# Optimization experiments

Hardware: AMD Instinct MI355X
Metric: run time of the kernel (lower is better)

The kernel has to match this reference:

```python
import jax, jax.numpy as jnp
import numpy as np

N, A, C = 4, 8732, 81
SCALE_XY, SCALE_WH = 0.1, 0.2   # dboxes.scale_xy / scale_wh; Loss uses reciprocals
LAM, W_IOU = 1.0, 0.01
EPS_IOU = float(np.finfo(float).eps)


def setup_inputs() -> dict:
    key = jax.random.key(0)
    ks = jax.random.split(key, 8)
    ploc = jax.random.normal(ks[0], (N, 4, A), dtype=jnp.float32) * 0.5
    plabel = jax.random.normal(ks[1], (N, C, A), dtype=jnp.float32)
    # ground-truth loc in xywh with strictly positive wh (loc_vec takes a log)
    gxy = jax.random.uniform(ks[2], (N, 2, A), dtype=jnp.float32)
    gwh = jax.random.uniform(ks[3], (N, 2, A), dtype=jnp.float32) * 0.4 + 0.05
    gloc = jnp.concatenate([gxy, gwh], axis=1)
    lab = jax.random.randint(ks[4], (N, A), 1, C)
    keep = jax.random.uniform(ks[5], (N, A)) < 0.02
    glabel = jnp.where(keep, lab, 0).astype(jnp.int32)
    # default boxes in xywh, shape [1, 4, A]
    dxy = jax.random.uniform(ks[6], (1, 2, A), dtype=jnp.float32)
    dwh = jax.random.uniform(ks[7], (1, 2, A), dtype=jnp.float32) * 0.45 + 0.05
    dboxes = jnp.concatenate([dxy, dwh], axis=1)
    return {"ploc": ploc, "plabel": plabel, "gloc": gloc, "glabel": glabel, "dboxes": dboxes}


def _decode_ltrb(loc, dboxes):
    """scale_back_batch: encoded [N,4,A] + dboxes xywh [1,4,A] -> ltrb [N,A,4]."""
    b = jnp.transpose(loc, (0, 2, 1))      # [N, A, 4]
    d = jnp.transpose(dboxes, (0, 2, 1))   # [1, A, 4]
    xy = SCALE_XY * b[..., :2] * d[..., 2:] + d[..., :2]
    wh = jnp.exp(SCALE_WH * b[..., 2:]) * d[..., 2:]
    return jnp.concatenate([xy - 0.5 * wh, xy + 0.5 * wh], axis=-1)


def _iou_sum(p, g):
    """p, g: [A,4] ltrb -> per-anchor sum over all g boxes of IoU(p_i, g_k)."""
    area_p = (p[:, 2] - p[:, 0]) * (p[:, 3] - p[:, 1])
    area_g = (g[:, 2] - g[:, 0]) * (g[:, 3] - g[:, 1])
    iw = jnp.maximum(jnp.minimum(p[:, None, 2], g[None, :, 2]) - jnp.maximum(p[:, None, 0], g[None, :, 0]), 0.0)
    ih = jnp.maximum(jnp.minimum(p[:, None, 3], g[None, :, 3]) - jnp.maximum(p[:, None, 1], g[None, :, 1]), 0.0)
    inter = iw * ih                                      # [A, A]
    ua = jnp.maximum(area_p[:, None] + area_g[None, :] - inter, EPS_IOU)
    return (inter / ua).sum(axis=1)                      # [A]


def _forward(ploc, plabel, gloc, glabel, dboxes):
    mask = glabel > 0                                    # [N, A]
    pos_num = mask.sum(axis=1)                           # [N]

    # loc_vec: encode ground truth against default boxes
    dxy, dwh = dboxes[:, :2, :], dboxes[:, 2:, :]
    gxy_t = (1.0 / SCALE_XY) * (gloc[:, :2, :] - dxy) / dwh
    gwh_t = (1.0 / SCALE_WH) * jnp.log(gloc[:, 2:, :] / dwh)
    vec_gd = jnp.concatenate([gxy_t, gwh_t], axis=1)     # [N, 4, A]

    # SmoothL1 (beta=1), summed over coord dim
    diff = ploc - vec_gd
    ad = jnp.abs(diff)
    sl1 = jnp.where(ad < 1.0, 0.5 * diff * diff, ad - 0.5).sum(axis=1)  # [N, A]

    # per-anchor cross entropy
    logp = jax.nn.log_softmax(plabel, axis=1)            # [N, C, A]
    con = -jnp.take_along_axis(logp, glabel[:, None, :], axis=1)[:, 0, :]  # [N, A]

    # weighted-IoU reweighting (weights are detached in the original)
    p_ltrb = _decode_ltrb(ploc, dboxes)                  # [N, A, 4]
    g_ltrb = _decode_ltrb(gloc, dboxes)
    iou_s = jax.vmap(_iou_sum)(p_ltrb, g_ltrb)           # [N, A]
    valid = (p_ltrb[..., 0] < p_ltrb[..., 2]) & (p_ltrb[..., 1] < p_ltrb[..., 3])
    weights = jnp.where(valid, W_IOU * iou_s ** LAM, 0.0)
    weights = jax.lax.stop_gradient(weights)
    sl1 = (sl1 / (sl1 + weights)) * sl1

    sl1_pos = (mask.astype(sl1.dtype) * sl1).sum(axis=1)  # [N]

    # hard negative mining: double argsort for ranks
    con_neg = jnp.where(mask, 0.0, con)
    con_idx = jnp.argsort(-con_neg, axis=1)
    con_rank = jnp.argsort(con_idx, axis=1)
    neg_num = jnp.minimum(3 * pos_num, A)[:, None]
    neg_mask = con_rank < neg_num
    closs = (con * (mask.astype(con.dtype) + neg_mask.astype(con.dtype))).sum(axis=1)

    total = sl1_pos + closs
    num_mask = (pos_num > 0).astype(total.dtype)
    pn = jnp.maximum(pos_num.astype(total.dtype), 1e-6)
    return (total * num_mask / pn).mean()


def reference(ploc, plabel, gloc, glabel, dboxes):
    return _forward(ploc, plabel, gloc, glabel, dboxes)
```

## Files before the change

kernel.cpp:

```cpp
#include <hip/hip_runtime.h>
#include <math.h>

#define A_N 8732
#define A4 2183
#define NAT (4 * A_N)
#define BATCH 4
#define CLS 81
#define TILE 256
#define NBINS 2048
#define HB 16
#define HCHUNK ((A_N + HB - 1) / HB)
#define CSPL 8
#define PLB 8

__device__ __forceinline__ float sl1f(float d) {
    float ad = fabsf(d);
    return ad < 1.0f ? 0.5f * d * d : ad - 0.5f;
}
__device__ __forceinline__ float fget(const float4& v, int j) {
    switch (j) { case 0: return v.x; case 1: return v.y; case 2: return v.z; default: return v.w; }
}
__device__ __forceinline__ unsigned umap(float v) {
    return __float_as_uint(v) | 0x80000000u;
}

__device__ void suffix_find(const int* lcnt, const float* lsum, int k, int tid,
                            int* ic, float* fsum,
                            int* o_b, int* o_krem, float* o_sumA)
{
    int base = tid * 8;
    int cs = 0; float ss = 0.0f;
    #pragma unroll
    for (int j = 0; j < 8; j++) { cs += lcnt[base + j]; ss += lsum[base + j]; }
    ic[tid] = cs; fsum[tid] = ss;
    __syncthreads();
    for (int off = 1; off < TILE; off <<= 1) {
        int v = ic[tid]; float f = fsum[tid];
        int v2 = 0; float f2 = 0.0f;
        if (tid + off < TILE) { v2 = ic[tid + off]; f2 = fsum[tid + off]; }
        __syncthreads();
        ic[tid] = v + v2; fsum[tid] = f + f2;
        __syncthreads();
    }
    int run = ic[tid] - cs;
    float runs = fsum[tid] - ss;
    for (int j = 7; j >= 0; j--) {
        int b = base + j; int c = lcnt[b];
        if (run < k && run + c >= k) { *o_b = b; *o_krem = k - run; *o_sumA = runs; }
        run += c; runs += lsum[b];
    }
    __syncthreads();
}

__global__ void init_kernel(int* h1cnt, float* h1sum, int* h2cnt, float* h2sum,
                            int* posnum, float* sums, float* out) {
    int idx = blockIdx.x * TILE + threadIdx.x;
    const int HN = BATCH * NBINS;
    if (idx < HN) { h1cnt[idx] = 0; h1sum[idx] = 0.0f; h2cnt[idx] = 0; h2sum[idx] = 0.0f; }
    if (idx < BATCH) posnum[idx] = 0;
    if (idx < 2 * BATCH) sums[idx] = 0.0f;
    if (idx == 0) out[0] = 0.0f;
}

__global__ __launch_bounds__(TILE) void prep_kernel(
    const float* __restrict__ ploc, const float* __restrict__ plabel,
    const float* __restrict__ gloc, const int* __restrict__ glabel,
    const float* __restrict__ dboxes,
    float4* __restrict__ pbox, float4* __restrict__ gbox,
    float4* __restrict__ sl1raw4, float* __restrict__ xg,
    float* __restrict__ separt,
    int* __restrict__ poslist, int* __restrict__ posnum)
{
    int a4 = blockIdx.x * TILE + threadIdx.x;
    int n = blockIdx.y, z = blockIdx.z;
    if (a4 >= A4) return;

    if (z < CSPL) {
        int c0 = z * 10, c1 = (z == CSPL - 1) ? CLS : c0 + 10;
        const float4* pb4 = (const float4*)plabel + (size_t)n * CLS * A4;
        float4 se = make_float4(0.f, 0.f, 0.f, 0.f);
        for (int c = c0; c < c1; c++) {
            float4 v = pb4[(size_t)c * A4 + a4];
            se.x += expf(v.x); se.y += expf(v.y); se.z += expf(v.z); se.w += expf(v.w);
        }
        ((float4*)(separt + (size_t)z * NAT + (size_t)n * A_N))[a4] = se;
        return;
    }

    const float4* pl4 = (const float4*)ploc + (size_t)n * 4 * A4;
    const float4* gl4 = (const float4*)gloc + (size_t)n * 4 * A4;
    const float4* db4 = (const float4*)dboxes;
    const int4*   lb4 = (const int4*)glabel + (size_t)n * A4;

    float4 dx = db4[0*A4+a4], dy = db4[1*A4+a4], dw = db4[2*A4+a4], dh = db4[3*A4+a4];
    float4 px = pl4[0*A4+a4], py = pl4[1*A4+a4], pw = pl4[2*A4+a4], ph = pl4[3*A4+a4];
    float4 gx = gl4[0*A4+a4], gy = gl4[1*A4+a4], gw = gl4[2*A4+a4], gh = gl4[3*A4+a4];
    int4 lab4 = lb4[a4];
    int labs[4] = {lab4.x, lab4.y, lab4.z, lab4.w};

    float slr[4];
    #pragma unroll
    for (int j = 0; j < 4; j++) {
        int a = 4 * a4 + j;
        float d0 = fget(dx,j), d1 = fget(dy,j), d2 = fget(dw,j), d3 = fget(dh,j);
        float p0 = fget(px,j), p1 = fget(py,j), p2 = fget(pw,j), p3 = fget(ph,j);
        float g0 = fget(gx,j), g1 = fget(gy,j), g2 = fget(gw,j), g3 = fget(gh,j);

        float v0 = 10.0f * (g0 - d0) / d2;
        float v1 = 10.0f * (g1 - d1) / d3;
        float v2 = 5.0f * logf(g2 / d2);
        float v3 = 5.0f * logf(g3 / d3);
        slr[j] = sl1f(p0-v0) + sl1f(p1-v1) + sl1f(p2-v2) + sl1f(p3-v3);

        float cx = 0.1f*p0*d2 + d0, cy = 0.1f*p1*d3 + d1;
        float cw = expf(0.2f*p2)*d2, ch = expf(0.2f*p3)*d3;
        pbox[(size_t)n*A_N + a] = make_float4(cx-0.5f*cw, cy-0.5f*ch, cx+0.5f*cw, cy+0.5f*ch);
        float ex = 0.1f*g0*d2 + d0, ey = 0.1f*g1*d3 + d1;
        float ew = expf(0.2f*g2)*d2, eh = expf(0.2f*g3)*d3;
        gbox[(size_t)n*A_N + a] = make_float4(ex-0.5f*ew, ey-0.5f*eh, ex+0.5f*ew, ey+0.5f*eh);

        int lab = labs[j];
        xg[n*A_N + a] = plabel[(size_t)n*CLS*A_N + (size_t)lab*A_N + a];
        if (lab > 0) {
            int pos = atomicAdd(&posnum[n], 1);
            poslist[n*A_N + pos] = a;
        }
    }
    sl1raw4[(size_t)n*A4 + a4] = make_float4(slr[0], slr[1], slr[2], slr[3]);
}

__global__ __launch_bounds__(TILE) void mid_kernel(
    const float* __restrict__ separt, const float* __restrict__ xg,
    const int* __restrict__ glabel,
    const float4* __restrict__ pbox, const float4* __restrict__ gbox,
    const float* __restrict__ sl1raw, const int* __restrict__ poslist,
    const int* __restrict__ posnum,
    float* __restrict__ conneg, float* __restrict__ sums,
    int* __restrict__ h1cnt, float* __restrict__ h1sum)
{
    __shared__ int   lcnt[NBINS];
    __shared__ float lsum[NBINS];
    __shared__ float r4[4];
    const int n = blockIdx.y, z = blockIdx.z, tid = threadIdx.x;

    if (z == 0) {
        for (int b = tid; b < NBINS; b += TILE) { lcnt[b] = 0; lsum[b] = 0.0f; }
        __syncthreads();
        int i0 = blockIdx.x * HCHUNK, i1 = min(A_N, i0 + HCHUNK);
        for (int i = i0 + tid; i < i1; i += TILE) {
            float se = 0.0f;
            #pragma unroll
            for (int z2 = 0; z2 < CSPL; z2++) se += separt[(size_t)z2 * NAT + n * A_N + i];
            float cv = logf(se) - xg[n * A_N + i];
            bool msk = glabel[n * A_N + i] > 0;
            float cng = msk ? 0.0f : cv;
            conneg[n * A_N + i] = cng;
            if (msk) atomicAdd(&sums[n], cv);
            int d = (umap(cng) >> 20) & (NBINS - 1);
            atomicAdd(&lcnt[d], 1);
            atomicAdd(&lsum[d], cng);
        }
        __syncthreads();
        for (int b = tid; b < NBINS; b += TILE)
            if (lcnt[b]) { atomicAdd(&h1cnt[n * NBINS + b], lcnt[b]); atomicAdd(&h1sum[n * NBINS + b], lsum[b]); }
    } else {
        int np = posnum[n];
        for (int p = (z - 1) * HB + blockIdx.x; p < np; p += HB * PLB) {
            int a = poslist[n * A_N + p];
            float4 b = pbox[(size_t)n * A_N + a];
            float ap = (b.z - b.x) * (b.w - b.y);
            float acc = 0.0f;
            for (int k = tid; k < A_N; k += TILE) {
                float4 g = gbox[(size_t)n * A_N + k];
                float iw = fmaxf(fminf(b.z, g.z) - fmaxf(b.x, g.x), 0.0f);
                float ih = fmaxf(fminf(b.w, g.w) - fmaxf(b.y, g.y), 0.0f);
                float inter = iw * ih;
                float ua = ap + (g.z - g.x) * (g.w - g.y) - inter;
                acc += inter * __builtin_amdgcn_rcpf(ua);
            }
            #pragma unroll
            for (int off = 32; off > 0; off >>= 1) acc += __shfl_down(acc, off);
            if ((tid & 63) == 0) r4[tid >> 6] = acc;
            __syncthreads();
            if (tid == 0) {
                float iou = r4[0] + r4[1] + r4[2] + r4[3];
                bool valid = (b.x < b.z) && (b.y < b.w);
                float w = valid ? 0.01f * iou : 0.0f;
                float s = sl1raw[n * A_N + a];
                atomicAdd(&sums[BATCH + n], s / (s + w) * s);
            }
            __syncthreads();
        }
    }
}

__global__ __launch_bounds__(TILE) void hist2_kernel(
    const float* __restrict__ conneg, const int* __restrict__ posnum,
    const int* __restrict__ h1cnt, const float* __restrict__ h1sum,
    int* __restrict__ h2cnt, float* __restrict__ h2sum)
{
    __shared__ int   lcnt[NBINS];
    __shared__ float lsum[NBINS];
    __shared__ int   ic[TILE];
    __shared__ float fs_[TILE];
    __shared__ int sb, skrem; __shared__ float ssA;
    const int n = blockIdx.y, tid = threadIdx.x;
    int np = posnum[n];
    if (np <= 0) return;
    int k = min(3 * np, A_N);

    for (int b = tid; b < NBINS; b += TILE) { lcnt[b] = h1cnt[n * NBINS + b]; lsum[b] = 0.0f; }
    __syncthreads();
    suffix_find(lcnt, lsum, k, tid, ic, fs_, &sb, &skrem, &ssA);
    int b1 = sb;
    __syncthreads();

    for (int b = tid; b < NBINS; b += TILE) { lcnt[b] = 0; lsum[b] = 0.0f; }
    __syncthreads();
    int i0 = blockIdx.x * HCHUNK, i1 = min(A_N, i0 + HCHUNK);
    for (int i = i0 + tid; i < i1; i += TILE) {
        float v = conneg[n * A_N + i];
        unsigned u = umap(v);
        if ((int)((u >> 20) & (NBINS - 1)) == b1) {
            int d = (u >> 9) & (NBINS - 1);
            atomicAdd(&lcnt[d], 1);
            atomicAdd(&lsum[d], v);
        }
    }
    __syncthreads();
    for (int b = tid; b < NBINS; b += TILE)
        if (lcnt[b]) { atomicAdd(&h2cnt[n * NBINS + b], lcnt[b]); atomicAdd(&h2sum[n * NBINS + b], lsum[b]); }
}

__global__ __launch_bounds__(TILE) void final_kernel(
    const int* __restrict__ h1cnt, const float* __restrict__ h1sum,
    const int* __restrict__ h2cnt, const float* __restrict__ h2sum,
    const int* __restrict__ posnum, const float* __restrict__ sums,
    float* __restrict__ out)
{
    __shared__ int   lcnt[NBINS];
    __shared__ float lsum[NBINS];
    __shared__ int   ic[TILE];
    __shared__ float fs_[TILE];
    __shared__ int sb1, skrem1, sb2, skrem2; __shared__ float ssA1, ssA2;
    const int n = blockIdx.x, tid = threadIdx.x;
    int np = posnum[n];
    if (np <= 0) return;
    int k = min(3 * np, A_N);

    for (int b = tid; b < NBINS; b += TILE) { lcnt[b] = h1cnt[n * NBINS + b]; lsum[b] = h1sum[n * NBINS + b]; }
    __syncthreads();
    suffix_find(lcnt, lsum, k, tid, ic, fs_, &sb1, &skrem1, &ssA1);

    for (int b = tid; b < NBINS; b += TILE) { lcnt[b] = h2cnt[n * NBINS + b]; lsum[b] = h2sum[n * NBINS + b]; }
    __syncthreads();
    suffix_find(lcnt, lsum, skrem1, tid, ic, fs_, &sb2, &skrem2, &ssA2);

    if (tid == 0) {
        unsigned ubin = ((unsigned)sb1 << 20) | ((unsigned)sb2 << 9) | 256u;
        float tval = __uint_as_float(ubin & 0x7fffffffu);
        float closs_neg = ssA1 + ssA2 + (float)skrem2 * tval;
        float tot = sums[n] + sums[BATCH + n] + closs_neg;
        atomicAdd(out, tot / (float)np * (1.0f / BATCH));
    }
}

extern "C" void kernel_launch(void* const* d_in, const int* in_sizes, int n_in,
                              void* d_out, int out_size, void* d_ws, size_t ws_size,
                              hipStream_t stream) {
    const float* ploc   = (const float*)d_in[0];
    const float* plabel = (const float*)d_in[1];
    const float* gloc   = (const float*)d_in[2];
    const int*   glabel = (const int*)d_in[3];
    const float* dboxes = (const float*)d_in[4];
    float* out = (float*)d_out;

    float* ws = (float*)d_ws;
    float4* pbox    = (float4*)ws;
    float4* gbox    = pbox + NAT;
    float*  sl1raw  = ws + 8 * (size_t)NAT;
    float*  conneg  = sl1raw + NAT;
    float*  xg      = conneg + NAT;
    float*  separt  = xg + NAT;
    int*    poslist = (int*)(separt + (size_t)CSPL * NAT);
    int*    posnum  = poslist + NAT;
    float*  sums    = (float*)(posnum + BATCH);
    int*    h1cnt   = (int*)(sums + 2 * BATCH);
    float*  h1sum   = (float*)(h1cnt + BATCH * NBINS);
    int*    h2cnt   = (int*)(h1sum + BATCH * NBINS);
    float*  h2sum   = (float*)(h2cnt + BATCH * NBINS);

    const int PBLK = (A4 + TILE - 1) / TILE;

    init_kernel<<<(BATCH * NBINS + TILE - 1) / TILE, TILE, 0, stream>>>(
        h1cnt, h1sum, h2cnt, h2sum, posnum, sums, out);
    prep_kernel<<<dim3(PBLK, BATCH, CSPL + 1), TILE, 0, stream>>>(
        ploc, plabel, gloc, glabel, dboxes,
        pbox, gbox, (float4*)sl1raw, xg, separt, poslist, posnum);
    mid_kernel<<<dim3(HB, BATCH, PLB + 1), TILE, 0, stream>>>(
        separt, xg, glabel, pbox, gbox, sl1raw, poslist, posnum,
        conneg, sums, h1cnt, h1sum);
    hist2_kernel<<<dim3(HB, BATCH), TILE, 0, stream>>>(
        conneg, posnum, h1cnt, h1sum, h2cnt, h2sum);
    final_kernel<<<BATCH, TILE, 0, stream>>>(
        h1cnt, h1sum, h2cnt, h2sum, posnum, sums, out);
}
```

Baseline: 114.5 us.

## Fuse five-kernel pipeline into prep and tail kernels with memset init

Measured after the change: 111.4 us. -2.8%, faster.

```diff
diff --git a/kernel.cpp b/kernel.cpp
--- a/kernel.cpp
+++ b/kernel.cpp
@@ -2,23 +2,16 @@
 #include <math.h>
 
 #define A_N 8732
-#define A4 2183
 #define NAT (4 * A_N)
 #define BATCH 4
 #define CLS 81
 #define TILE 256
 #define NBINS 2048
-#define HB 16
-#define HCHUNK ((A_N + HB - 1) / HB)
-#define CSPL 8
-#define PLB 8
+#define PLB 128
 
 __device__ __forceinline__ float sl1f(float d) {
     float ad = fabsf(d);
     return ad < 1.0f ? 0.5f * d * d : ad - 0.5f;
-}
-__device__ __forceinline__ float fget(const float4& v, int j) {
-    switch (j) { case 0: return v.x; case 1: return v.y; case 2: return v.z; default: return v.w; }
 }
 __device__ __forceinline__ unsigned umap(float v) {
     return __float_as_uint(v) | 0x80000000u;
@@ -52,65 +45,54 @@
     __syncthreads();
 }
 
-__global__ void init_kernel(int* h1cnt, float* h1sum, int* h2cnt, float* h2sum,
-                            int* posnum, float* sums, float* out) {
-    int idx = blockIdx.x * TILE + threadIdx.x;
-    const int HN = BATCH * NBINS;
-    if (idx < HN) { h1cnt[idx] = 0; h1sum[idx] = 0.0f; h2cnt[idx] = 0; h2sum[idx] = 0.0f; }
-    if (idx < BATCH) posnum[idx] = 0;
-    if (idx < 2 * BATCH) sums[idx] = 0.0f;
-    if (idx == 0) out[0] = 0.0f;
-}
-
 __global__ __launch_bounds__(TILE) void prep_kernel(
     const float* __restrict__ ploc, const float* __restrict__ plabel,
     const float* __restrict__ gloc, const int* __restrict__ glabel,
     const float* __restrict__ dboxes,
     float4* __restrict__ pbox, float4* __restrict__ gbox,
-    float4* __restrict__ sl1raw4, float* __restrict__ xg,
-    float* __restrict__ separt,
-    int* __restrict__ poslist, int* __restrict__ posnum)
+    float* __restrict__ sl1raw, float* __restrict__ conneg,
+    int* __restrict__ poslist, int* __restrict__ posnum,
+    float* __restrict__ sums, int* __restrict__ h1cnt, float* __restrict__ h1sum)
 {
-    int a4 = blockIdx.x * TILE + threadIdx.x;
-    int n = blockIdx.y, z = blockIdx.z;
-    if (a4 >= A4) return;
-
-    if (z < CSPL) {
-        int c0 = z * 10, c1 = (z == CSPL - 1) ? CLS : c0 + 10;
-        const float4* pb4 = (const float4*)plabel + (size_t)n * CLS * A4;
-        float4 se = make_float4(0.f, 0.f, 0.f, 0.f);
-        for (int c = c0; c < c1; c++) {
-            float4 v = pb4[(size_t)c * A4 + a4];
-            se.x += expf(v.x); se.y += expf(v.y); se.z += expf(v.z); se.w += expf(v.w);
-        }
-        ((float4*)(separt + (size_t)z * NAT + (size_t)n * A_N))[a4] = se;
-        return;
-    }
-
-    const float4* pl4 = (const float4*)ploc + (size_t)n * 4 * A4;
-    const float4* gl4 = (const float4*)gloc + (size_t)n * 4 * A4;
-    const float4* db4 = (const float4*)dboxes;
-    const int4*   lb4 = (const int4*)glabel + (size_t)n * A4;
-
-    float4 dx = db4[0*A4+a4], dy = db4[1*A4+a4], dw = db4[2*A4+a4], dh = db4[3*A4+a4];
-    float4 px = pl4[0*A4+a4], py = pl4[1*A4+a4], pw = pl4[2*A4+a4], ph = pl4[3*A4+a4];
-    float4 gx = gl4[0*A4+a4], gy = gl4[1*A4+a4], gw = gl4[2*A4+a4], gh = gl4[3*A4+a4];
-    int4 lab4 = lb4[a4];
-    int labs[4] = {lab4.x, lab4.y, lab4.z, lab4.w};
-
-    float slr[4];
-    #pragma unroll
-    for (int j = 0; j < 4; j++) {
-        int a = 4 * a4 + j;
-        float d0 = fget(dx,j), d1 = fget(dy,j), d2 = fget(dw,j), d3 = fget(dh,j);
-        float p0 = fget(px,j), p1 = fget(py,j), p2 = fget(pw,j), p3 = fget(ph,j);
-        float g0 = fget(gx,j), g1 = fget(gy,j), g2 = fget(gw,j), g3 = fget(gh,j);
+    __shared__ int   lcnt[NBINS];
+    __shared__ float lsum[NBINS];
+    const int tid = threadIdx.x;
+    const int a = blockIdx.x * TILE + tid;
+    const int n = blockIdx.y;
+    for (int b = tid; b < NBINS; b += TILE) { lcnt[b] = 0; lsum[b] = 0.0f; }
+    __syncthreads();
+
+    if (a < A_N) {
+        const float* pb = plabel + (size_t)n * CLS * A_N + a;
+        float se = 0.0f;
+        #pragma unroll 27
+        for (int c = 0; c < CLS; c++) se += expf(pb[(size_t)c * A_N]);
+        int lab = glabel[n * A_N + a];
+        float xg = pb[(size_t)lab * A_N];
+        float cv = logf(se) - xg;
+        bool msk = lab > 0;
+        float cng = msk ? 0.0f : cv;
+        conneg[n * A_N + a] = cng;
+        if (msk) {
+            int pos = atomicAdd(&posnum[n], 1);
+            poslist[n * A_N + pos] = a;
+            atomicAdd(&sums[n], cv);
+        }
+        int d = (umap(cng) >> 20) & (NBINS - 1);
+        atomicAdd(&lcnt[d], 1);
+        atomicAdd(&lsum[d], cng);
+
+        float d0 = dboxes[0*A_N+a], d1 = dboxes[1*A_N+a], d2 = dboxes[2*A_N+a], d3 = dboxes[3*A_N+a];
+        const float* pl = ploc + (size_t)n * 4 * A_N;
+        const float* gl = gloc + (size_t)n * 4 * A_N;
+        float p0 = pl[0*A_N+a], p1 = pl[1*A_N+a], p2 = pl[2*A_N+a], p3 = pl[3*A_N+a];
+        float g0 = gl[0*A_N+a], g1 = gl[1*A_N+a], g2 = gl[2*A_N+a], g3 = gl[3*A_N+a];
 
         float v0 = 10.0f * (g0 - d0) / d2;
         float v1 = 10.0f * (g1 - d1) / d3;
         float v2 = 5.0f * logf(g2 / d2);
         float v3 = 5.0f * logf(g3 / d3);
-        slr[j] = sl1f(p0-v0) + sl1f(p1-v1) + sl1f(p2-v2) + sl1f(p3-v3);
+        sl1raw[n * A_N + a] = sl1f(p0-v0) + sl1f(p1-v1) + sl1f(p2-v2) + sl1f(p3-v3);
 
         float cx = 0.1f*p0*d2 + d0, cy = 0.1f*p1*d3 + d1;
         float cw = expf(0.2f*p2)*d2, ch = expf(0.2f*p3)*d3;
@@ -118,54 +100,34 @@
         float ex = 0.1f*g0*d2 + d0, ey = 0.1f*g1*d3 + d1;
         float ew = expf(0.2f*g2)*d2, eh = expf(0.2f*g3)*d3;
         gbox[(size_t)n*A_N + a] = make_float4(ex-0.5f*ew, ey-0.5f*eh, ex+0.5f*ew, ey+0.5f*eh);
-
-        int lab = labs[j];
-        xg[n*A_N + a] = plabel[(size_t)n*CLS*A_N + (size_t)lab*A_N + a];
-        if (lab > 0) {
-            int pos = atomicAdd(&posnum[n], 1);
-            poslist[n*A_N + pos] = a;
-        }
-    }
-    sl1raw4[(size_t)n*A4 + a4] = make_float4(slr[0], slr[1], slr[2], slr[3]);
-}
-
-__global__ __launch_bounds__(TILE) void mid_kernel(
-    const float* __restrict__ separt, const float* __restrict__ xg,
-    const int* __restrict__ glabel,
+    }
+    __syncthreads();
+    for (int b = tid; b < NBINS; b += TILE)
+        if (lcnt[b]) { atomicAdd(&h1cnt[n * NBINS + b], lcnt[b]); atomicAdd(&h1sum[n * NBINS + b], lsum[b]); }
+}
+
+__global__ __launch_bounds__(TILE) void tail_kernel(
     const float4* __restrict__ pbox, const float4* __restrict__ gbox,
-    const float* __restrict__ sl1raw, const int* __restrict__ poslist,
-    const int* __restrict__ posnum,
-    float* __restrict__ conneg, float* __restrict__ sums,
-    int* __restrict__ h1cnt, float* __restrict__ h1sum)
+    const float* __restrict__ sl1raw, const float* __restrict__ conneg,
+    const int* __restrict__ poslist, const int* __restrict__ posnum,
+    const float* __restrict__ sums,
+    const int* __restrict__ h1cnt, const float* __restrict__ h1sum,
+    float* __restrict__ out)
 {
     __shared__ int   lcnt[NBINS];
     __shared__ float lsum[NBINS];
+    __shared__ int   ic[TILE];
+    __shared__ float fs_[TILE];
+    __shared__ int sb1, skrem1, sb2, skrem2;
+    __shared__ float ssA1, ssA2;
     __shared__ float r4[4];
-    const int n = blockIdx.y, z = blockIdx.z, tid = threadIdx.x;
-
-    if (z == 0) {
-        for (int b = tid; b < NBINS; b += TILE) { lcnt[b] = 0; lsum[b] = 0.0f; }
-        __syncthreads();
-        int i0 = blockIdx.x * HCHUNK, i1 = min(A_N, i0 + HCHUNK);
-        for (int i = i0 + tid; i < i1; i += TILE) {
-            float se = 0.0f;
-            #pragma unroll
-            for (int z2 = 0; z2 < CSPL; z2++) se += separt[(size_t)z2 * NAT + n * A_N + i];
-            float cv = logf(se) - xg[n * A_N + i];
-            bool msk = glabel[n * A_N + i] > 0;
-            float cng = msk ? 0.0f : cv;
-            conneg[n * A_N + i] = cng;
-            if (msk) atomicAdd(&sums[n], cv);
-            int d = (umap(cng) >> 20) & (NBINS - 1);
-            atomicAdd(&lcnt[d], 1);
-            atomicAdd(&lsum[d], cng);
-        }
-        __syncthreads();
-        for (int b = tid; b < NBINS; b += TILE)
-            if (lcnt[b]) { atomicAdd(&h1cnt[n * NBINS + b], lcnt[b]); atomicAdd(&h1sum[n * NBINS + b], lsum[b]); }
-    } else {
-        int np = posnum[n];
-        for (int p = (z - 1) * HB + blockIdx.x; p < np; p += HB * PLB) {
+    const int n = blockIdx.y, tid = threadIdx.x;
+    const int np = posnum[n];
+    if (np <= 0) return;
+    const float inv = 1.0f / ((float)np * (float)BATCH);
+
+    if (blockIdx.x < PLB) {
+        for (int p = blockIdx.x; p < np; p += PLB) {
             int a = poslist[n * A_N + p];
             float4 b = pbox[(size_t)n * A_N + a];
             float ap = (b.z - b.x) * (b.w - b.y);
@@ -187,81 +149,38 @@
                 bool valid = (b.x < b.z) && (b.y < b.w);
                 float w = valid ? 0.01f * iou : 0.0f;
                 float s = sl1raw[n * A_N + a];
-                atomicAdd(&sums[BATCH + n], s / (s + w) * s);
+                atomicAdd(out, (s / (s + w) * s) * inv);
             }
             __syncthreads();
         }
-    }
-}
-
-__global__ __launch_bounds__(TILE) void hist2_kernel(
-    const float* __restrict__ conneg, const int* __restrict__ posnum,
-    const int* __restrict__ h1cnt, const float* __restrict__ h1sum,
-    int* __restrict__ h2cnt, float* __restrict__ h2sum)
-{
-    __shared__ int   lcnt[NBINS];
-    __shared__ float lsum[NBINS];
-    __shared__ int   ic[TILE];
-    __shared__ float fs_[TILE];
-    __shared__ int sb, skrem; __shared__ float ssA;
-    const int n = blockIdx.y, tid = threadIdx.x;
-    int np = posnum[n];
-    if (np <= 0) return;
-    int k = min(3 * np, A_N);
-
-    for (int b = tid; b < NBINS; b += TILE) { lcnt[b] = h1cnt[n * NBINS + b]; lsum[b] = 0.0f; }
-    __syncthreads();
-    suffix_find(lcnt, lsum, k, tid, ic, fs_, &sb, &skrem, &ssA);
-    int b1 = sb;
-    __syncthreads();
-
-    for (int b = tid; b < NBINS; b += TILE) { lcnt[b] = 0; lsum[b] = 0.0f; }
-    __syncthreads();
-    int i0 = blockIdx.x * HCHUNK, i1 = min(A_N, i0 + HCHUNK);
-    for (int i = i0 + tid; i < i1; i += TILE) {
-        float v = conneg[n * A_N + i];
-        unsigned u = umap(v);
-        if ((int)((u >> 20) & (NBINS - 1)) == b1) {
-            int d = (u >> 9) & (NBINS - 1);
-            atomicAdd(&lcnt[d], 1);
-            atomicAdd(&lsum[d], v);
-        }
-    }
-    __syncthreads();
-    for (int b = tid; b < NBINS; b += TILE)
-        if (lcnt[b]) { atomicAdd(&h2cnt[n * NBINS + b], lcnt[b]); atomicAdd(&h2sum[n * NBINS + b], lsum[b]); }
-}
-
-__global__ __launch_bounds__(TILE) void final_kernel(
-    const int* __restrict__ h1cnt, const float* __restrict__ h1sum,
-    const int* __restrict__ h2cnt, const float* __restrict__ h2sum,
-    const int* __restrict__ posnum, const float* __restrict__ sums,
-    float* __restrict__ out)
-{
-    __shared__ int   lcnt[NBINS];
-    __shared__ float lsum[NBINS];
-    __shared__ int   ic[TILE];
-    __shared__ float fs_[TILE];
-    __shared__ int sb1, skrem1, sb2, skrem2; __shared__ float ssA1, ssA2;
-    const int n = blockIdx.x, tid = threadIdx.x;
-    int np = posnum[n];
-    if (np <= 0) return;
-    int k = min(3 * np, A_N);
-
-    for (int b = tid; b < NBINS; b += TILE) { lcnt[b] = h1cnt[n * NBINS + b]; lsum[b] = h1sum[n * NBINS + b]; }
-    __syncthreads();
-    suffix_find(lcnt, lsum, k, tid, ic, fs_, &sb1, &skrem1, &ssA1);
-
-    for (int b = tid; b < NBINS; b += TILE) { lcnt[b] = h2cnt[n * NBINS + b]; lsum[b] = h2sum[n * NBINS + b]; }
-    __syncthreads();
-    suffix_find(lcnt, lsum, skrem1, tid, ic, fs_, &sb2, &skrem2, &ssA2);
-
-    if (tid == 0) {
-        unsigned ubin = ((unsigned)sb1 << 20) | ((unsigned)sb2 << 9) | 256u;
-        float tval = __uint_as_float(ubin & 0x7fffffffu);
-        float closs_neg = ssA1 + ssA2 + (float)skrem2 * tval;
-        float tot = sums[n] + sums[BATCH + n] + closs_neg;
-        atomicAdd(out, tot / (float)np * (1.0f / BATCH));
+    } else {
+        int k = min(3 * np, A_N);
+        for (int b = tid; b < NBINS; b += TILE) { lcnt[b] = h1cnt[n * NBINS + b]; lsum[b] = h1sum[n * NBINS + b]; }
+        __syncthreads();
+        suffix_find(lcnt, lsum, k, tid, ic, fs_, &sb1, &skrem1, &ssA1);
+        int b1 = sb1;
+        __syncthreads();
+
+        for (int b = tid; b < NBINS; b += TILE) { lcnt[b] = 0; lsum[b] = 0.0f; }
+        __syncthreads();
+        for (int i = tid; i < A_N; i += TILE) {
+            float v = conneg[n * A_N + i];
+            unsigned u = umap(v);
+            if ((int)((u >> 20) & (NBINS - 1)) == b1) {
+                int d = (u >> 9) & (NBINS - 1);
+                atomicAdd(&lcnt[d], 1);
+                atomicAdd(&lsum[d], v);
+            }
+        }
+        __syncthreads();
+        suffix_find(lcnt, lsum, skrem1, tid, ic, fs_, &sb2, &skrem2, &ssA2);
+
+        if (tid == 0) {
+            unsigned ubin = 0x80000000u | ((unsigned)sb1 << 20) | ((unsigned)sb2 << 9) | 256u;
+            float tval = __uint_as_float(ubin & 0x7fffffffu);
+            float closs_neg = ssA1 + ssA2 + (float)skrem2 * tval;
+            atomicAdd(out, (sums[n] + closs_neg) * inv);
+        }
     }
 }
 
@@ -275,33 +194,23 @@
     const float* dboxes = (const float*)d_in[4];
     float* out = (float*)d_out;
 
-    float* ws = (float*)d_ws;
-    float4* pbox    = (float4*)ws;
-    float4* gbox    = pbox + NAT;
-    float*  sl1raw  = ws + 8 * (size_t)NAT;
-    float*  conneg  = sl1raw + NAT;
-    float*  xg      = conneg + NAT;
-    float*  separt  = xg + NAT;
-    int*    poslist = (int*)(separt + (size_t)CSPL * NAT);
-    int*    posnum  = poslist + NAT;
-    float*  sums    = (float*)(posnum + BATCH);
-    int*    h1cnt   = (int*)(sums + 2 * BATCH);
-    float*  h1sum   = (float*)(h1cnt + BATCH * NBINS);
-    int*    h2cnt   = (int*)(h1sum + BATCH * NBINS);
-    float*  h2sum   = (float*)(h2cnt + BATCH * NBINS);
-
-    const int PBLK = (A4 + TILE - 1) / TILE;
-
-    init_kernel<<<(BATCH * NBINS + TILE - 1) / TILE, TILE, 0, stream>>>(
-        h1cnt, h1sum, h2cnt, h2sum, posnum, sums, out);
-    prep_kernel<<<dim3(PBLK, BATCH, CSPL + 1), TILE, 0, stream>>>(
+    int*    h1cnt  = (int*)d_ws;
+    float*  h1sum  = (float*)(h1cnt + BATCH * NBINS);
+    int*    posnum = (int*)(h1sum + BATCH * NBINS);
+    float*  sums   = (float*)(posnum + BATCH);
+    float4* pbox   = (float4*)(sums + BATCH);
+    float4* gbox   = pbox + NAT;
+    float*  sl1raw = (float*)(gbox + NAT);
+    float*  conneg = sl1raw + NAT;
+    int*    poslist = (int*)(conneg + NAT);
+
+    const size_t zbytes = (size_t)(2 * BATCH * NBINS + 2 * BATCH) * 4;
+
+    hipMemsetAsync(d_ws, 0, zbytes, stream);
+    hipMemsetAsync(d_out, 0, sizeof(float), stream);
+    prep_kernel<<<dim3((A_N + TILE - 1) / TILE, BATCH), TILE, 0, stream>>>(
         ploc, plabel, gloc, glabel, dboxes,
-        pbox, gbox, (float4*)sl1raw, xg, separt, poslist, posnum);
-    mid_kernel<<<dim3(HB, BATCH, PLB + 1), TILE, 0, stream>>>(
-        separt, xg, glabel, pbox, gbox, sl1raw, poslist, posnum,
-        conneg, sums, h1cnt, h1sum);
-    hist2_kernel<<<dim3(HB, BATCH), TILE, 0, stream>>>(
-        conneg, posnum, h1cnt, h1sum, h2cnt, h2sum);
-    final_kernel<<<BATCH, TILE, 0, stream>>>(
-        h1cnt, h1sum, h2cnt, h2sum, posnum, sums, out);
-}
+        pbox, gbox, sl1raw, conneg, poslist, posnum, sums, h1cnt, h1sum);
+    tail_kernel<<<dim3(PLB + 1, BATCH), TILE, 0, stream>>>(
+        pbox, gbox, sl1raw, conneg, poslist, posnum, sums, h1cnt, h1sum, out);
+}
```
